# Kernel tuning notes

Hardware: AMD Instinct MI355X
Metric: run time of the kernel (lower is better)

## Reference

```python
import jax, jax.numpy as jnp
import numpy as np

CLIP_TANH = 10.0
M_CHECKS, N_VARS = 256, 512   # parity-check matrix shape
ROW_W = 8                     # ones per check row -> E = 256*8 = 2048 edges
BATCH = 16384


def _build_masks():
    """Tanner-graph connectivity masks, as in init_w_skipconn2even / initialize_w_v2c."""
    rng = np.random.default_rng(0)
    pcm = np.zeros((M_CHECKS, N_VARS), np.float32)
    for r in range(M_CHECKS):
        pcm[r, rng.choice(N_VARS, ROW_W, replace=False)] = 1.0
    checks, variables = np.nonzero(pcm)  # edge list, row-major order, length E
    E = checks.size
    # edge e' feeds edge e iff same variable node, different check node
    same_var = variables[:, None] == variables[None, :]
    diff_chk = checks[:, None] != checks[None, :]
    w_odd2even_mask = (same_var & diff_chk).astype(np.float32)               # [E, E]
    # variable v feeds every edge incident to it
    w_skip_mask = (np.arange(N_VARS)[:, None] == variables[None, :]).astype(np.float32)  # [N, E]
    return jnp.asarray(w_odd2even_mask), jnp.asarray(w_skip_mask), E


def setup_inputs() -> dict:
    key = jax.random.key(0)
    w_o2e_mask, w_skip_mask, E = _build_masks()
    k = jax.random.split(key, 5)
    return {
        "x": jax.random.normal(k[0], (BATCH, E), jnp.float32),          # edge messages
        "llr": jax.random.normal(k[1], (BATCH, N_VARS), jnp.float32),   # channel LLRs
        "u": jax.random.uniform(k[2], (E,), jnp.float32),               # dropout uniforms
        "odd_weights": 0.05 * jax.random.normal(k[3], (E, E), jnp.float32),
        "llr_weights": 1.0 + 0.05 * jax.random.normal(k[4], (N_VARS, E), jnp.float32),
        "dropout_logits": 10.0 * jnp.ones((E,), jnp.float32),           # 10000*LOGITS_INIT analogue (sigmoid ~ 1)
        "w_odd2even_mask": w_o2e_mask,
        "w_skipconn2even_mask": w_skip_mask,
    }


def reference(x, llr, u, odd_weights, llr_weights, dropout_logits,
              w_odd2even_mask, w_skipconn2even_mask):
    # TEST-phase forward, mask_only=False
    total_mask = w_odd2even_mask * odd_weights                        # [E, E], very sparse support
    z = (u < jax.nn.sigmoid(dropout_logits)).astype(x.dtype)          # Bernoulli gate per source edge
    mask_after_dropout = total_mask * z[:, None]                      # row-wise gating
    msg = x @ mask_after_dropout                                      # [B, E]
    skip = llr @ (w_skipconn2even_mask * llr_weights)                 # [B, E]
    odd_clamp = jnp.clip(msg + skip, -CLIP_TANH, CLIP_TANH)
    return jnp.tanh(0.5 * odd_clamp)
```

## Files before the change

### kernel.cpp

```cpp
#include <hip/hip_runtime.h>
#include <hip/hip_bf16.h>

constexpr int E     = 2048;
constexpr int NVARS = 512;
constexpr int DMAX  = 20;
constexpr int TB    = 8;
constexpr int NT    = 512;

__device__ __forceinline__ unsigned bf16hi(float f) {
    const unsigned uu = __float_as_uint(f);
    return (uu + 0x7FFFu + ((uu >> 16) & 1u)) & 0xFFFF0000u;
}
__device__ __forceinline__ unsigned cvtpk(float lo, float hi) {
    unsigned r;
    asm("v_cvt_pk_bf16_f32 %0, %1, %2" : "=v"(r) : "v"(lo), "v"(hi));
    return r;
}
__device__ __forceinline__ float bl(unsigned q) { return __uint_as_float(q << 16); }
__device__ __forceinline__ float bh(unsigned q) { return __uint_as_float(q & 0xFFFF0000u); }

__global__ __launch_bounds__(256)
void k_vsrc(const float* __restrict__ skip_mask,
            const float* __restrict__ llr_w,
            unsigned short* __restrict__ vsrc,
            float* __restrict__ skw)
{
    const int col = blockIdx.x * 256 + threadIdx.x;
    const int v0  = blockIdx.y * (NVARS / 32);
    for (int v = v0; v < v0 + NVARS / 32; ++v) {
        const float m = skip_mask[(size_t)v * E + col];
        if (m != 0.0f) {
            vsrc[col] = (unsigned short)v;
            skw [col] = m * llr_w[(size_t)v * E + col];
        }
    }
}

__global__ __launch_bounds__(64)
void k_pervar(const unsigned short* __restrict__ vsrc,
              const float* __restrict__ skw,
              const float* __restrict__ odd_w,
              const float* __restrict__ u,
              const float* __restrict__ logits,
              uint4*  __restrict__ wtc,
              float4* __restrict__ hdr,
              int*    __restrict__ nitems)
{
    __shared__ unsigned short vs[E];
    __shared__ int deg[NVARS];
    __shared__ unsigned short mem[DMAX];
    __shared__ float zf[DMAX];
    __shared__ float sks[DMAX];

    const int v   = blockIdx.x;
    const int tid = threadIdx.x;

    for (int i = tid; i < E / 8; i += 64)
        ((uint4*)vs)[i] = ((const uint4*)vsrc)[i];
    for (int i = tid; i < NVARS; i += 64) deg[i] = 0;
    __syncthreads();
    for (int i = tid; i < E; i += 64) atomicAdd(&deg[vs[i]], 1);
    __syncthreads();

    const int dv = deg[v];

    int itot = 0, ib = 0, wb = 0;
    for (int i = tid; i < NVARS; i += 64) {
        const int d2 = deg[i];
        if (!d2) continue;
        const int dc = (d2 < DMAX) ? d2 : DMAX;
        const int ic = (dc + 3) >> 2;
        itot += ic;
        if (dv > 0 && (d2 < dv || (d2 == dv && i < v))) { ib += ic; wb += dc * ic; }
    }
    #pragma unroll
    for (int o = 32; o; o >>= 1) {
        itot += __shfl_xor(itot, o);
        ib   += __shfl_xor(ib,   o);
        wb   += __shfl_xor(wb,   o);
    }
    if (v == 0 && tid == 0) nitems[0] = itot;
    if (!dv) return;
    const int de = (dv < DMAX) ? dv : DMAX;
    const int ic = (de + 3) >> 2;

    int cnt = 0;
    for (int c = 0; c < E / 64; ++c) {
        const int e = c * 64 + tid;
        const bool m = ((int)vs[e] == v);
        const unsigned long long bal = __ballot(m);
        if (m) {
            const int pos = cnt + __popcll(bal & ((1ull << tid) - 1ull));
            if (pos < DMAX) mem[pos] = (unsigned short)e;
        }
        cnt += __popcll(bal);
    }
    __syncthreads();

    if (tid < de) {
        const int m = mem[tid];
        const float sig = 1.0f / (1.0f + __expf(-logits[m]));
        zf [tid] = (u[m] < sig) ? 1.0f : 0.0f;
        sks[tid] = skw[m];
    }
    __syncthreads();

    if (tid < ic) {
        const int o0 = tid * 4;
        float s0 = 0, s1 = 0, s2 = 0, s3 = 0;
        unsigned c0 = 0xFFFFu, c1 = 0xFFFFu, c2 = 0xFFFFu, c3 = 0xFFFFu;
        if (o0 + 0 < de) { s0 = sks[o0 + 0]; c0 = mem[o0 + 0]; }
        if (o0 + 1 < de) { s1 = sks[o0 + 1]; c1 = mem[o0 + 1]; }
        if (o0 + 2 < de) { s2 = sks[o0 + 2]; c2 = mem[o0 + 2]; }
        if (o0 + 3 < de) { s3 = sks[o0 + 3]; c3 = mem[o0 + 3]; }
        hdr[2 * (ib + tid)]     = make_float4(s0, s1, s2, s3);
        hdr[2 * (ib + tid) + 1] = make_float4(
            __uint_as_float(c0 | (c1 << 16)),
            __uint_as_float(c2 | (c3 << 16)),
            __uint_as_float((unsigned)(wb + tid * de)),
            __uint_as_float((unsigned)v | ((unsigned)de << 16)));
    }

    for (int idx = tid; idx < de * ic; idx += 64) {
        const int k = idx / de;
        const int j = idx - k * de;
        const int src = mem[j];
        unsigned g[4];
        #pragma unroll
        for (int q = 0; q < 4; ++q) {
            const int o = 4 * k + q;
            float ww = 0.0f;
            if (o < de && o != j)
                ww = odd_w[(size_t)src * E + mem[o]] * zf[j];
            g[q] = bf16hi(ww) | (unsigned)src;
        }
        wtc[wb + idx] = make_uint4(g[0], g[1], g[2], g[3]);
    }
}

__device__ __forceinline__ float th(float s) {
    float c = fminf(fmaxf(s, -10.0f), 10.0f);
    float t = __expf(c);
    return (t - 1.0f) * __builtin_amdgcn_rcpf(t + 1.0f);
}

#define FMA8(gq, xvq)                                                         \
    {                                                                         \
        const float w0 = bh((gq).x), w1 = bh((gq).y);                         \
        const float w2 = bh((gq).z), w3 = bh((gq).w);                         \
        const float xf0 = bl((xvq).x), xf1 = bh((xvq).x);                     \
        const float xf2 = bl((xvq).y), xf3 = bh((xvq).y);                     \
        const float xf4 = bl((xvq).z), xf5 = bh((xvq).z);                     \
        const float xf6 = bl((xvq).w), xf7 = bh((xvq).w);                     \
        a[0][0] += w0 * xf0; a[0][1] += w0 * xf1;                             \
        a[0][2] += w0 * xf2; a[0][3] += w0 * xf3;                             \
        a[0][4] += w0 * xf4; a[0][5] += w0 * xf5;                             \
        a[0][6] += w0 * xf6; a[0][7] += w0 * xf7;                             \
        a[1][0] += w1 * xf0; a[1][1] += w1 * xf1;                             \
        a[1][2] += w1 * xf2; a[1][3] += w1 * xf3;                             \
        a[1][4] += w1 * xf4; a[1][5] += w1 * xf5;                             \
        a[1][6] += w1 * xf6; a[1][7] += w1 * xf7;                             \
        a[2][0] += w2 * xf0; a[2][1] += w2 * xf1;                             \
        a[2][2] += w2 * xf2; a[2][3] += w2 * xf3;                             \
        a[2][4] += w2 * xf4; a[2][5] += w2 * xf5;                             \
        a[2][6] += w2 * xf6; a[2][7] += w2 * xf7;                             \
        a[3][0] += w3 * xf0; a[3][1] += w3 * xf1;                             \
        a[3][2] += w3 * xf2; a[3][3] += w3 * xf3;                             \
        a[3][4] += w3 * xf4; a[3][5] += w3 * xf5;                             \
        a[3][6] += w3 * xf6; a[3][7] += w3 * xf7;                             \
    }

__global__ __launch_bounds__(NT, 6)
void fused_main(const float* __restrict__ x,
                const float* __restrict__ llr,
                const uint4*  __restrict__ wtc,
                const float4* __restrict__ hdr,
                const int*    __restrict__ nitems,
                float* __restrict__ out)
{
    __shared__ uint4 xs[E];
    __shared__ uint4 ls[NVARS];

    const int b0 = blockIdx.x * TB;
    const int t  = threadIdx.x;
    const int nit = nitems[0];

    const float4* xr = (const float4*)(x + (size_t)b0 * E);
    const float4 r0 = xr[0 * (E / 4) + t];
    const float4 r1 = xr[1 * (E / 4) + t];
    const float4 r2 = xr[2 * (E / 4) + t];
    const float4 r3 = xr[3 * (E / 4) + t];
    const float4 r4 = xr[4 * (E / 4) + t];
    const float4 r5 = xr[5 * (E / 4) + t];
    const float4 r6 = xr[6 * (E / 4) + t];
    const float4 r7 = xr[7 * (E / 4) + t];
    const float* lr = llr + (size_t)b0 * NVARS;
    const float l0 = lr[t],             l1 = lr[NVARS + t];
    const float l2 = lr[2 * NVARS + t], l3 = lr[3 * NVARS + t];
    const float l4 = lr[4 * NVARS + t], l5 = lr[5 * NVARS + t];
    const float l6 = lr[6 * NVARS + t], l7 = lr[7 * NVARS + t];

    const float4 ha0 = hdr[2 * t];
    const uint4  hb0 = ((const uint4*)hdr)[2 * t + 1];
    const uint4* wp0 = wtc + hb0.z;
    const uint4  g00 = wp0[0];
    const uint4  g01 = wp0[1];

    xs[4 * t + 0] = make_uint4(cvtpk(r0.x, r1.x), cvtpk(r2.x, r3.x),
                               cvtpk(r4.x, r5.x), cvtpk(r6.x, r7.x));
    xs[4 * t + 1] = make_uint4(cvtpk(r0.y, r1.y), cvtpk(r2.y, r3.y),
                               cvtpk(r4.y, r5.y), cvtpk(r6.y, r7.y));
    xs[4 * t + 2] = make_uint4(cvtpk(r0.z, r1.z), cvtpk(r2.z, r3.z),
                               cvtpk(r4.z, r5.z), cvtpk(r6.z, r7.z));
    xs[4 * t + 3] = make_uint4(cvtpk(r0.w, r1.w), cvtpk(r2.w, r3.w),
                               cvtpk(r4.w, r5.w), cvtpk(r6.w, r7.w));
    ls[t] = make_uint4(cvtpk(l0, l1), cvtpk(l2, l3),
                       cvtpk(l4, l5), cvtpk(l6, l7));
    __syncthreads();

    unsigned sst[2][4][4];
    unsigned scc[2][2];

    {
        const int v = hb0.w & 0xFFFF;
        const int d = hb0.w >> 16;

        const uint4 lvq = ls[v];
        const float lf0 = bl(lvq.x), lf1 = bh(lvq.x);
        const float lf2 = bl(lvq.y), lf3 = bh(lvq.y);
        const float lf4 = bl(lvq.z), lf5 = bh(lvq.z);
        const float lf6 = bl(lvq.w), lf7 = bh(lvq.w);

        float a[4][8];
        #pragma unroll
        for (int ii = 0; ii < 4; ++ii) {
            const float sk = (ii == 0) ? ha0.x : (ii == 1) ? ha0.y
                           : (ii == 2) ? ha0.z : ha0.w;
            a[ii][0] = sk * lf0; a[ii][1] = sk * lf1;
            a[ii][2] = sk * lf2; a[ii][3] = sk * lf3;
            a[ii][4] = sk * lf4; a[ii][5] = sk * lf5;
            a[ii][6] = sk * lf6; a[ii][7] = sk * lf7;
        }

        uint4 gc = g00, gn = g01;
        uint4 xc = xs[gc.x & 0x7FFu];
        for (int j = 0; j < d - 1; ++j) {
            const uint4 gf = wp0[j + 2];
            const uint4 xn = xs[gn.x & 0x7FFu];
            FMA8(gc, xc);
            gc = gn; xc = xn; gn = gf;
        }
        FMA8(gc, xc);

        scc[0][0] = hb0.x;
        scc[0][1] = hb0.y;
        #pragma unroll
        for (int ii = 0; ii < 4; ++ii) {
            sst[0][ii][0] = cvtpk(th(a[ii][0]), th(a[ii][1]));
            sst[0][ii][1] = cvtpk(th(a[ii][2]), th(a[ii][3]));
            sst[0][ii][2] = cvtpk(th(a[ii][4]), th(a[ii][5]));
            sst[0][ii][3] = cvtpk(th(a[ii][6]), th(a[ii][7]));
        }
    }

    scc[1][0] = 0xFFFFFFFFu;
    scc[1][1] = 0xFFFFFFFFu;
    if (NT + t < nit) {
        const int it = NT + t;
        const float4 ha1 = hdr[2 * it];
        const uint4  hb1 = ((const uint4*)hdr)[2 * it + 1];
        const uint4* wp1 = wtc + hb1.z;
        const int v = hb1.w & 0xFFFF;
        const int d = hb1.w >> 16;

        const uint4 lvq = ls[v];
        const float lf0 = bl(lvq.x), lf1 = bh(lvq.x);
        const float lf2 = bl(lvq.y), lf3 = bh(lvq.y);
        const float lf4 = bl(lvq.z), lf5 = bh(lvq.z);
        const float lf6 = bl(lvq.w), lf7 = bh(lvq.w);

        float a[4][8];
        #pragma unroll
        for (int ii = 0; ii < 4; ++ii) {
            const float sk = (ii == 0) ? ha1.x : (ii == 1) ? ha1.y
                           : (ii == 2) ? ha1.z : ha1.w;
            a[ii][0] = sk * lf0; a[ii][1] = sk * lf1;
            a[ii][2] = sk * lf2; a[ii][3] = sk * lf3;
            a[ii][4] = sk * lf4; a[ii][5] = sk * lf5;
            a[ii][6] = sk * lf6; a[ii][7] = sk * lf7;
        }

        uint4 gc = wp1[0], gn = wp1[1];
        uint4 xc = xs[gc.x & 0x7FFu];
        for (int j = 0; j < d - 1; ++j) {
            const uint4 gf = wp1[j + 2];
            const uint4 xn = xs[gn.x & 0x7FFu];
            FMA8(gc, xc);
            gc = gn; xc = xn; gn = gf;
        }
        FMA8(gc, xc);

        scc[1][0] = hb1.x;
        scc[1][1] = hb1.y;
        #pragma unroll
        for (int ii = 0; ii < 4; ++ii) {
            sst[1][ii][0] = cvtpk(th(a[ii][0]), th(a[ii][1]));
            sst[1][ii][1] = cvtpk(th(a[ii][2]), th(a[ii][3]));
            sst[1][ii][2] = cvtpk(th(a[ii][4]), th(a[ii][5]));
            sst[1][ii][3] = cvtpk(th(a[ii][6]), th(a[ii][7]));
        }
    }

    __syncthreads();
    unsigned* osp = (unsigned*)xs;
    #pragma unroll
    for (int r = 0; r < 2; ++r) {
        #pragma unroll
        for (int ii = 0; ii < 4; ++ii) {
            const unsigned c = (scc[r][ii >> 1] >> ((ii & 1) * 16)) & 0xFFFFu;
            if (c != 0xFFFFu) {
                osp[0 * E + c] = sst[r][ii][0];
                osp[1 * E + c] = sst[r][ii][1];
                osp[2 * E + c] = sst[r][ii][2];
                osp[3 * E + c] = sst[r][ii][3];
            }
        }
    }
    __syncthreads();

    {
        const int row = t >> 6, l = t & 63;
        const int p = row >> 1, hf = row & 1;
        float* orow = out + (size_t)(b0 + row) * E;
        const uint4* plane = (const uint4*)(osp + p * E);
        #pragma unroll
        for (int i = 0; i < 8; ++i) {
            const int q4 = i * 64 + l;
            const uint4 w4 = plane[q4];
            float4 o;
            if (hf == 0)
                o = make_float4(bl(w4.x), bl(w4.y), bl(w4.z), bl(w4.w));
            else
                o = make_float4(bh(w4.x), bh(w4.y), bh(w4.z), bh(w4.w));
            ((float4*)orow)[q4] = o;
        }
    }
}

extern "C" void kernel_launch(void* const* d_in, const int* in_sizes, int n_in,
                              void* d_out, int out_size, void* d_ws, size_t ws_size,
                              hipStream_t stream) {
    const float* x        = (const float*)d_in[0];
    const float* llr      = (const float*)d_in[1];
    const float* u        = (const float*)d_in[2];
    const float* odd_w    = (const float*)d_in[3];
    const float* llr_w    = (const float*)d_in[4];
    const float* logits   = (const float*)d_in[5];
    const float* skip_msk = (const float*)d_in[7];
    float* out = (float*)d_out;

    const int B = in_sizes[0] / E;

    char* wsb = (char*)d_ws;
    size_t off = 0;
    uint4*          wtc  = (uint4*)(wsb + off);          off += (size_t)6144 * 16;
    float4*         hdr  = (float4*)(wsb + off);         off += (size_t)1024 * 32;
    float*          skw  = (float*)(wsb + off);          off += (size_t)E * 4;
    unsigned short* vsrc = (unsigned short*)(wsb + off); off += (size_t)E * 2;
    int*            nit  = (int*)(wsb + off);            off += 16;

    k_vsrc  <<<dim3(E / 256, 32), dim3(256), 0, stream>>>(skip_msk, llr_w, vsrc, skw);
    k_pervar<<<dim3(NVARS),       dim3(64),  0, stream>>>(vsrc, skw, odd_w, u, logits,
                                                          wtc, hdr, nit);

    fused_main<<<dim3(B / TB), dim3(NT), 0, stream>>>(x, llr, wtc, hdr, nit, out);
}
```

Measured before the change: 96.74 us.

## Process two batch tiles per block and prefetch the second tile's x during compute

The grid is halved so each block handles two 8-row batch tiles in sequence. The x rows for the second tile are loaded into registers right after the first tile is staged in LDS, so that global load overlaps the first tile's gather/FMA compute. This trades occupancy and parallelism (half as many blocks, more live registers) for latency hiding. It also hardcodes the batch size (16384) instead of deriving it from the input size.

```diff
diff --git a/kernel.cpp b/kernel.cpp
--- a/kernel.cpp
+++ b/kernel.cpp
@@ -6,6 +6,8 @@
 constexpr int DMAX  = 20;
 constexpr int TB    = 8;
 constexpr int NT    = 512;
+constexpr int NTILE = 16384 / TB;
+constexpr int GRID  = NTILE / 2;
 
 __device__ __forceinline__ unsigned bf16hi(float f) {
     const unsigned uu = __float_as_uint(f);
@@ -181,169 +183,176 @@
     __shared__ uint4 xs[E];
     __shared__ uint4 ls[NVARS];
 
-    const int b0 = blockIdx.x * TB;
-    const int t  = threadIdx.x;
+    const int t   = threadIdx.x;
     const int nit = nitems[0];
 
-    const float4* xr = (const float4*)(x + (size_t)b0 * E);
-    const float4 r0 = xr[0 * (E / 4) + t];
-    const float4 r1 = xr[1 * (E / 4) + t];
-    const float4 r2 = xr[2 * (E / 4) + t];
-    const float4 r3 = xr[3 * (E / 4) + t];
-    const float4 r4 = xr[4 * (E / 4) + t];
-    const float4 r5 = xr[5 * (E / 4) + t];
-    const float4 r6 = xr[6 * (E / 4) + t];
-    const float4 r7 = xr[7 * (E / 4) + t];
-    const float* lr = llr + (size_t)b0 * NVARS;
-    const float l0 = lr[t],             l1 = lr[NVARS + t];
-    const float l2 = lr[2 * NVARS + t], l3 = lr[3 * NVARS + t];
-    const float l4 = lr[4 * NVARS + t], l5 = lr[5 * NVARS + t];
-    const float l6 = lr[6 * NVARS + t], l7 = lr[7 * NVARS + t];
-
-    const float4 ha0 = hdr[2 * t];
-    const uint4  hb0 = ((const uint4*)hdr)[2 * t + 1];
-    const uint4* wp0 = wtc + hb0.z;
-    const uint4  g00 = wp0[0];
-    const uint4  g01 = wp0[1];
-
-    xs[4 * t + 0] = make_uint4(cvtpk(r0.x, r1.x), cvtpk(r2.x, r3.x),
-                               cvtpk(r4.x, r5.x), cvtpk(r6.x, r7.x));
-    xs[4 * t + 1] = make_uint4(cvtpk(r0.y, r1.y), cvtpk(r2.y, r3.y),
-                               cvtpk(r4.y, r5.y), cvtpk(r6.y, r7.y));
-    xs[4 * t + 2] = make_uint4(cvtpk(r0.z, r1.z), cvtpk(r2.z, r3.z),
-                               cvtpk(r4.z, r5.z), cvtpk(r6.z, r7.z));
-    xs[4 * t + 3] = make_uint4(cvtpk(r0.w, r1.w), cvtpk(r2.w, r3.w),
-                               cvtpk(r4.w, r5.w), cvtpk(r6.w, r7.w));
-    ls[t] = make_uint4(cvtpk(l0, l1), cvtpk(l2, l3),
-                       cvtpk(l4, l5), cvtpk(l6, l7));
-    __syncthreads();
-
-    unsigned sst[2][4][4];
-    unsigned scc[2][2];
-
+    float4 rx[8];
     {
-        const int v = hb0.w & 0xFFFF;
-        const int d = hb0.w >> 16;
-
-        const uint4 lvq = ls[v];
-        const float lf0 = bl(lvq.x), lf1 = bh(lvq.x);
-        const float lf2 = bl(lvq.y), lf3 = bh(lvq.y);
-        const float lf4 = bl(lvq.z), lf5 = bh(lvq.z);
-        const float lf6 = bl(lvq.w), lf7 = bh(lvq.w);
-
-        float a[4][8];
+        const float4* xr = (const float4*)(x + (size_t)blockIdx.x * TB * E);
         #pragma unroll
-        for (int ii = 0; ii < 4; ++ii) {
-            const float sk = (ii == 0) ? ha0.x : (ii == 1) ? ha0.y
-                           : (ii == 2) ? ha0.z : ha0.w;
-            a[ii][0] = sk * lf0; a[ii][1] = sk * lf1;
-            a[ii][2] = sk * lf2; a[ii][3] = sk * lf3;
-            a[ii][4] = sk * lf4; a[ii][5] = sk * lf5;
-            a[ii][6] = sk * lf6; a[ii][7] = sk * lf7;
-        }
-
-        uint4 gc = g00, gn = g01;
-        uint4 xc = xs[gc.x & 0x7FFu];
-        for (int j = 0; j < d - 1; ++j) {
-            const uint4 gf = wp0[j + 2];
-            const uint4 xn = xs[gn.x & 0x7FFu];
+        for (int i = 0; i < 8; ++i) rx[i] = xr[i * (E / 4) + t];
+    }
+
+    #pragma unroll 1
+    for (int rep = 0; rep < 2; ++rep) {
+        const int b0 = (blockIdx.x + rep * GRID) * TB;
+
+        const float* lr = llr + (size_t)b0 * NVARS;
+        const float rl0 = lr[t],             rl1 = lr[NVARS + t];
+        const float rl2 = lr[2 * NVARS + t], rl3 = lr[3 * NVARS + t];
+        const float rl4 = lr[4 * NVARS + t], rl5 = lr[5 * NVARS + t];
+        const float rl6 = lr[6 * NVARS + t], rl7 = lr[7 * NVARS + t];
+
+        xs[4 * t + 0] = make_uint4(cvtpk(rx[0].x, rx[1].x), cvtpk(rx[2].x, rx[3].x),
+                                   cvtpk(rx[4].x, rx[5].x), cvtpk(rx[6].x, rx[7].x));
+        xs[4 * t + 1] = make_uint4(cvtpk(rx[0].y, rx[1].y), cvtpk(rx[2].y, rx[3].y),
+                                   cvtpk(rx[4].y, rx[5].y), cvtpk(rx[6].y, rx[7].y));
+        xs[4 * t + 2] = make_uint4(cvtpk(rx[0].z, rx[1].z), cvtpk(rx[2].z, rx[3].z),
+                                   cvtpk(rx[4].z, rx[5].z), cvtpk(rx[6].z, rx[7].z));
+        xs[4 * t + 3] = make_uint4(cvtpk(rx[0].w, rx[1].w), cvtpk(rx[2].w, rx[3].w),
+                                   cvtpk(rx[4].w, rx[5].w), cvtpk(rx[6].w, rx[7].w));
+        ls[t] = make_uint4(cvtpk(rl0, rl1), cvtpk(rl2, rl3),
+                           cvtpk(rl4, rl5), cvtpk(rl6, rl7));
+        __syncthreads();
+
+        if (rep == 0) {
+            const float4* xr2 = (const float4*)(x + (size_t)(b0 + GRID * TB) * E);
+            #pragma unroll
+            for (int i = 0; i < 8; ++i) rx[i] = xr2[i * (E / 4) + t];
+            __builtin_amdgcn_sched_barrier(0);
+        }
+
+        unsigned sst[2][4][4];
+        unsigned scc[2][2];
+
+        {
+            const float4 ha0 = hdr[2 * t];
+            const uint4  hb0 = ((const uint4*)hdr)[2 * t + 1];
+            const uint4* wp0 = wtc + hb0.z;
+            const int v = hb0.w & 0xFFFF;
+            const int d = hb0.w >> 16;
+
+            const uint4 lvq = ls[v];
+            const float lf0 = bl(lvq.x), lf1 = bh(lvq.x);
+            const float lf2 = bl(lvq.y), lf3 = bh(lvq.y);
+            const float lf4 = bl(lvq.z), lf5 = bh(lvq.z);
+            const float lf6 = bl(lvq.w), lf7 = bh(lvq.w);
+
+            float a[4][8];
+            #pragma unroll
+            for (int ii = 0; ii < 4; ++ii) {
+                const float sk = (ii == 0) ? ha0.x : (ii == 1) ? ha0.y
+                               : (ii == 2) ? ha0.z : ha0.w;
+                a[ii][0] = sk * lf0; a[ii][1] = sk * lf1;
+                a[ii][2] = sk * lf2; a[ii][3] = sk * lf3;
+                a[ii][4] = sk * lf4; a[ii][5] = sk * lf5;
+                a[ii][6] = sk * lf6; a[ii][7] = sk * lf7;
+            }
+
+            uint4 gc = wp0[0], gn = wp0[1];
+            uint4 xc = xs[gc.x & 0x7FFu];
+            for (int j = 0; j < d - 1; ++j) {
+                const uint4 gf = wp0[j + 2];
+                const uint4 xn = xs[gn.x & 0x7FFu];
+                FMA8(gc, xc);
+                gc = gn; xc = xn; gn = gf;
+            }
             FMA8(gc, xc);
-            gc = gn; xc = xn; gn = gf;
-        }
-        FMA8(gc, xc);
-
-        scc[0][0] = hb0.x;
-        scc[0][1] = hb0.y;
+
+            scc[0][0] = hb0.x;
+            scc[0][1] = hb0.y;
+            #pragma unroll
+            for (int ii = 0; ii < 4; ++ii) {
+                sst[0][ii][0] = cvtpk(th(a[ii][0]), th(a[ii][1]));
+                sst[0][ii][1] = cvtpk(th(a[ii][2]), th(a[ii][3]));
+                sst[0][ii][2] = cvtpk(th(a[ii][4]), th(a[ii][5]));
+                sst[0][ii][3] = cvtpk(th(a[ii][6]), th(a[ii][7]));
+            }
+        }
+
+        scc[1][0] = 0xFFFFFFFFu;
+        scc[1][1] = 0xFFFFFFFFu;
+        if (NT + t < nit) {
+            const int it = NT + t;
+            const float4 ha1 = hdr[2 * it];
+            const uint4  hb1 = ((const uint4*)hdr)[2 * it + 1];
+            const uint4* wp1 = wtc + hb1.z;
+            const int v = hb1.w & 0xFFFF;
+            const int d = hb1.w >> 16;
+
+            const uint4 lvq = ls[v];
+            const float lf0 = bl(lvq.x), lf1 = bh(lvq.x);
+            const float lf2 = bl(lvq.y), lf3 = bh(lvq.y);
+            const float lf4 = bl(lvq.z), lf5 = bh(lvq.z);
+            const float lf6 = bl(lvq.w), lf7 = bh(lvq.w);
+
+            float a[4][8];
+            #pragma unroll
+            for (int ii = 0; ii < 4; ++ii) {
+                const float sk = (ii == 0) ? ha1.x : (ii == 1) ? ha1.y
+                               : (ii == 2) ? ha1.z : ha1.w;
+                a[ii][0] = sk * lf0; a[ii][1] = sk * lf1;
+                a[ii][2] = sk * lf2; a[ii][3] = sk * lf3;
+                a[ii][4] = sk * lf4; a[ii][5] = sk * lf5;
+                a[ii][6] = sk * lf6; a[ii][7] = sk * lf7;
+            }
+
+            uint4 gc = wp1[0], gn = wp1[1];
+            uint4 xc = xs[gc.x & 0x7FFu];
+            for (int j = 0; j < d - 1; ++j) {
+                const uint4 gf = wp1[j + 2];
+                const uint4 xn = xs[gn.x & 0x7FFu];
+                FMA8(gc, xc);
+                gc = gn; xc = xn; gn = gf;
+            }
+            FMA8(gc, xc);
+
+            scc[1][0] = hb1.x;
+            scc[1][1] = hb1.y;
+            #pragma unroll
+            for (int ii = 0; ii < 4; ++ii) {
+                sst[1][ii][0] = cvtpk(th(a[ii][0]), th(a[ii][1]));
+                sst[1][ii][1] = cvtpk(th(a[ii][2]), th(a[ii][3]));
+                sst[1][ii][2] = cvtpk(th(a[ii][4]), th(a[ii][5]));
+                sst[1][ii][3] = cvtpk(th(a[ii][6]), th(a[ii][7]));
+            }
+        }
+
+        __syncthreads();
+        unsigned* osp = (unsigned*)xs;
         #pragma unroll
-        for (int ii = 0; ii < 4; ++ii) {
-            sst[0][ii][0] = cvtpk(th(a[ii][0]), th(a[ii][1]));
-            sst[0][ii][1] = cvtpk(th(a[ii][2]), th(a[ii][3]));
-            sst[0][ii][2] = cvtpk(th(a[ii][4]), th(a[ii][5]));
-            sst[0][ii][3] = cvtpk(th(a[ii][6]), th(a[ii][7]));
-        }
-    }
-
-    scc[1][0] = 0xFFFFFFFFu;
-    scc[1][1] = 0xFFFFFFFFu;
-    if (NT + t < nit) {
-        const int it = NT + t;
-        const float4 ha1 = hdr[2 * it];
-        const uint4  hb1 = ((const uint4*)hdr)[2 * it + 1];
-        const uint4* wp1 = wtc + hb1.z;
-        const int v = hb1.w & 0xFFFF;
-        const int d = hb1.w >> 16;
-
-        const uint4 lvq = ls[v];
-        const float lf0 = bl(lvq.x), lf1 = bh(lvq.x);
-        const float lf2 = bl(lvq.y), lf3 = bh(lvq.y);
-        const float lf4 = bl(lvq.z), lf5 = bh(lvq.z);
-        const float lf6 = bl(lvq.w), lf7 = bh(lvq.w);
-
-        float a[4][8];
-        #pragma unroll
-        for (int ii = 0; ii < 4; ++ii) {
-            const float sk = (ii == 0) ? ha1.x : (ii == 1) ? ha1.y
-                           : (ii == 2) ? ha1.z : ha1.w;
-            a[ii][0] = sk * lf0; a[ii][1] = sk * lf1;
-            a[ii][2] = sk * lf2; a[ii][3] = sk * lf3;
-            a[ii][4] = sk * lf4; a[ii][5] = sk * lf5;
-            a[ii][6] = sk * lf6; a[ii][7] = sk * lf7;
-        }
-
-        uint4 gc = wp1[0], gn = wp1[1];
-        uint4 xc = xs[gc.x & 0x7FFu];
-        for (int j = 0; j < d - 1; ++j) {
-            const uint4 gf = wp1[j + 2];
-            const uint4 xn = xs[gn.x & 0x7FFu];
-            FMA8(gc, xc);
-            gc = gn; xc = xn; gn = gf;
-        }
-        FMA8(gc, xc);
-
-        scc[1][0] = hb1.x;
-        scc[1][1] = hb1.y;
-        #pragma unroll
-        for (int ii = 0; ii < 4; ++ii) {
-            sst[1][ii][0] = cvtpk(th(a[ii][0]), th(a[ii][1]));
-            sst[1][ii][1] = cvtpk(th(a[ii][2]), th(a[ii][3]));
-            sst[1][ii][2] = cvtpk(th(a[ii][4]), th(a[ii][5]));
-            sst[1][ii][3] = cvtpk(th(a[ii][6]), th(a[ii][7]));
-        }
-    }
-
-    __syncthreads();
-    unsigned* osp = (unsigned*)xs;
-    #pragma unroll
-    for (int r = 0; r < 2; ++r) {
-        #pragma unroll
-        for (int ii = 0; ii < 4; ++ii) {
-            const unsigned c = (scc[r][ii >> 1] >> ((ii & 1) * 16)) & 0xFFFFu;
-            if (c != 0xFFFFu) {
-                osp[0 * E + c] = sst[r][ii][0];
-                osp[1 * E + c] = sst[r][ii][1];
-                osp[2 * E + c] = sst[r][ii][2];
-                osp[3 * E + c] = sst[r][ii][3];
-            }
-        }
-    }
-    __syncthreads();
-
-    {
-        const int row = t >> 6, l = t & 63;
-        const int p = row >> 1, hf = row & 1;
-        float* orow = out + (size_t)(b0 + row) * E;
-        const uint4* plane = (const uint4*)(osp + p * E);
-        #pragma unroll
-        for (int i = 0; i < 8; ++i) {
-            const int q4 = i * 64 + l;
-            const uint4 w4 = plane[q4];
-            float4 o;
-            if (hf == 0)
-                o = make_float4(bl(w4.x), bl(w4.y), bl(w4.z), bl(w4.w));
-            else
-                o = make_float4(bh(w4.x), bh(w4.y), bh(w4.z), bh(w4.w));
-            ((float4*)orow)[q4] = o;
-        }
+        for (int r = 0; r < 2; ++r) {
+            #pragma unroll
+            for (int ii = 0; ii < 4; ++ii) {
+                const unsigned c = (scc[r][ii >> 1] >> ((ii & 1) * 16)) & 0xFFFFu;
+                if (c != 0xFFFFu) {
+                    osp[0 * E + c] = sst[r][ii][0];
+                    osp[1 * E + c] = sst[r][ii][1];
+                    osp[2 * E + c] = sst[r][ii][2];
+                    osp[3 * E + c] = sst[r][ii][3];
+                }
+            }
+        }
+        __syncthreads();
+
+        {
+            const int row = t >> 6, l = t & 63;
+            const int p = row >> 1, hf = row & 1;
+            float* orow = out + (size_t)(b0 + row) * E;
+            const uint4* plane = (const uint4*)(osp + p * E);
+            #pragma unroll
+            for (int i = 0; i < 8; ++i) {
+                const int q4 = i * 64 + l;
+                const uint4 w4 = plane[q4];
+                float4 o;
+                if (hf == 0)
+                    o = make_float4(bl(w4.x), bl(w4.y), bl(w4.z), bl(w4.w));
+                else
+                    o = make_float4(bh(w4.x), bh(w4.y), bh(w4.z), bh(w4.w));
+                ((float4*)orow)[q4] = o;
+            }
+        }
+        __syncthreads();
     }
 }
 
@@ -359,8 +368,6 @@
     const float* skip_msk = (const float*)d_in[7];
     float* out = (float*)d_out;
 
-    const int B = in_sizes[0] / E;
-
     char* wsb = (char*)d_ws;
     size_t off = 0;
     uint4*          wtc  = (uint4*)(wsb + off);          off += (size_t)6144 * 16;
@@ -373,5 +380,5 @@
     k_pervar<<<dim3(NVARS),       dim3(64),  0, stream>>>(vsrc, skw, odd_w, u, logits,
                                                           wtc, hdr, nit);
 
-    fused_main<<<dim3(B / TB), dim3(NT), 0, stream>>>(x, llr, wtc, hdr, nit, out);
-}
+    fused_main<<<dim3(GRID), dim3(NT), 0, stream>>>(x, llr, wtc, hdr, nit, out);
+}
```

Result: slower. 181.5 us (+87.6%).

## Split batch tile into two halves to overlap x loads and output stores with gather

Applied to the files above, without the earlier changes.

The 8-row batch tile is processed as two 4-row halves held in separate shared buffers. Loads of the second half's x rows are issued after the first gather, and the first half's outputs are written before the second gather runs. The aim is to hide global load and store latency behind compute and to shrink the accumulator register footprint from 32 to 16 floats. In exchange, the sparse weight stream and headers are walked twice per block, and extra barriers are added.

```diff
diff --git a/kernel.cpp b/kernel.cpp
--- a/kernel.cpp
+++ b/kernel.cpp
@@ -144,31 +144,63 @@
     return (t - 1.0f) * __builtin_amdgcn_rcpf(t + 1.0f);
 }
 
-#define FMA8(gq, xvq)                                                         \
+#define FMA4(gq, xv2)                                                         \
     {                                                                         \
         const float w0 = bh((gq).x), w1 = bh((gq).y);                         \
         const float w2 = bh((gq).z), w3 = bh((gq).w);                         \
-        const float xf0 = bl((xvq).x), xf1 = bh((xvq).x);                     \
-        const float xf2 = bl((xvq).y), xf3 = bh((xvq).y);                     \
-        const float xf4 = bl((xvq).z), xf5 = bh((xvq).z);                     \
-        const float xf6 = bl((xvq).w), xf7 = bh((xvq).w);                     \
+        const float xf0 = bl((xv2).x), xf1 = bh((xv2).x);                     \
+        const float xf2 = bl((xv2).y), xf3 = bh((xv2).y);                     \
         a[0][0] += w0 * xf0; a[0][1] += w0 * xf1;                             \
         a[0][2] += w0 * xf2; a[0][3] += w0 * xf3;                             \
-        a[0][4] += w0 * xf4; a[0][5] += w0 * xf5;                             \
-        a[0][6] += w0 * xf6; a[0][7] += w0 * xf7;                             \
         a[1][0] += w1 * xf0; a[1][1] += w1 * xf1;                             \
         a[1][2] += w1 * xf2; a[1][3] += w1 * xf3;                             \
-        a[1][4] += w1 * xf4; a[1][5] += w1 * xf5;                             \
-        a[1][6] += w1 * xf6; a[1][7] += w1 * xf7;                             \
         a[2][0] += w2 * xf0; a[2][1] += w2 * xf1;                             \
         a[2][2] += w2 * xf2; a[2][3] += w2 * xf3;                             \
-        a[2][4] += w2 * xf4; a[2][5] += w2 * xf5;                             \
-        a[2][6] += w2 * xf6; a[2][7] += w2 * xf7;                             \
         a[3][0] += w3 * xf0; a[3][1] += w3 * xf1;                             \
         a[3][2] += w3 * xf2; a[3][3] += w3 * xf3;                             \
-        a[3][4] += w3 * xf4; a[3][5] += w3 * xf5;                             \
-        a[3][6] += w3 * xf6; a[3][7] += w3 * xf7;                             \
-    }
+    }
+
+template<int HI>
+__device__ __forceinline__ void gather_item(
+    const uint2* __restrict__ xsh, const uint4* __restrict__ lsq,
+    const uint4* __restrict__ wtc, const float4 ha, const uint4 hb,
+    unsigned st[4][2])
+{
+    const uint4* wp = wtc + hb.z;
+    const int v = hb.w & 0xFFFF;
+    const int d = hb.w >> 16;
+
+    const uint4 lvq = lsq[v];
+    const unsigned lp0 = HI ? lvq.z : lvq.x;
+    const unsigned lp1 = HI ? lvq.w : lvq.y;
+    const float lf0 = bl(lp0), lf1 = bh(lp0);
+    const float lf2 = bl(lp1), lf3 = bh(lp1);
+
+    float a[4][4];
+    #pragma unroll
+    for (int ii = 0; ii < 4; ++ii) {
+        const float sk = (ii == 0) ? ha.x : (ii == 1) ? ha.y
+                       : (ii == 2) ? ha.z : ha.w;
+        a[ii][0] = sk * lf0; a[ii][1] = sk * lf1;
+        a[ii][2] = sk * lf2; a[ii][3] = sk * lf3;
+    }
+
+    uint4 gc = wp[0], gn = wp[1];
+    uint2 xc = xsh[gc.x & 0x7FFu];
+    for (int j = 0; j < d - 1; ++j) {
+        const uint4 gf = wp[j + 2];
+        const uint2 xn = xsh[gn.x & 0x7FFu];
+        FMA4(gc, xc);
+        gc = gn; xc = xn; gn = gf;
+    }
+    FMA4(gc, xc);
+
+    #pragma unroll
+    for (int ii = 0; ii < 4; ++ii) {
+        st[ii][0] = cvtpk(th(a[ii][0]), th(a[ii][1]));
+        st[ii][1] = cvtpk(th(a[ii][2]), th(a[ii][3]));
+    }
+}
 
 __global__ __launch_bounds__(NT, 6)
 void fused_main(const float* __restrict__ x,
@@ -178,7 +210,8 @@
                 const int*    __restrict__ nitems,
                 float* __restrict__ out)
 {
-    __shared__ uint4 xs[E];
+    __shared__ uint2 xsA[E];
+    __shared__ uint2 xsB[E];
     __shared__ uint4 ls[NVARS];
 
     const int b0 = blockIdx.x * TB;
@@ -190,10 +223,6 @@
     const float4 r1 = xr[1 * (E / 4) + t];
     const float4 r2 = xr[2 * (E / 4) + t];
     const float4 r3 = xr[3 * (E / 4) + t];
-    const float4 r4 = xr[4 * (E / 4) + t];
-    const float4 r5 = xr[5 * (E / 4) + t];
-    const float4 r6 = xr[6 * (E / 4) + t];
-    const float4 r7 = xr[7 * (E / 4) + t];
     const float* lr = llr + (size_t)b0 * NVARS;
     const float l0 = lr[t],             l1 = lr[NVARS + t];
     const float l2 = lr[2 * NVARS + t], l3 = lr[3 * NVARS + t];
@@ -202,146 +231,103 @@
 
     const float4 ha0 = hdr[2 * t];
     const uint4  hb0 = ((const uint4*)hdr)[2 * t + 1];
-    const uint4* wp0 = wtc + hb0.z;
-    const uint4  g00 = wp0[0];
-    const uint4  g01 = wp0[1];
-
-    xs[4 * t + 0] = make_uint4(cvtpk(r0.x, r1.x), cvtpk(r2.x, r3.x),
-                               cvtpk(r4.x, r5.x), cvtpk(r6.x, r7.x));
-    xs[4 * t + 1] = make_uint4(cvtpk(r0.y, r1.y), cvtpk(r2.y, r3.y),
-                               cvtpk(r4.y, r5.y), cvtpk(r6.y, r7.y));
-    xs[4 * t + 2] = make_uint4(cvtpk(r0.z, r1.z), cvtpk(r2.z, r3.z),
-                               cvtpk(r4.z, r5.z), cvtpk(r6.z, r7.z));
-    xs[4 * t + 3] = make_uint4(cvtpk(r0.w, r1.w), cvtpk(r2.w, r3.w),
-                               cvtpk(r4.w, r5.w), cvtpk(r6.w, r7.w));
+
+    xsA[4 * t + 0] = make_uint2(cvtpk(r0.x, r1.x), cvtpk(r2.x, r3.x));
+    xsA[4 * t + 1] = make_uint2(cvtpk(r0.y, r1.y), cvtpk(r2.y, r3.y));
+    xsA[4 * t + 2] = make_uint2(cvtpk(r0.z, r1.z), cvtpk(r2.z, r3.z));
+    xsA[4 * t + 3] = make_uint2(cvtpk(r0.w, r1.w), cvtpk(r2.w, r3.w));
     ls[t] = make_uint4(cvtpk(l0, l1), cvtpk(l2, l3),
                        cvtpk(l4, l5), cvtpk(l6, l7));
     __syncthreads();
 
-    unsigned sst[2][4][4];
-    unsigned scc[2][2];
+    unsigned st0[4][2], st1[4][2];
+    unsigned scc0x = hb0.x, scc0y = hb0.y;
+    unsigned scc1x = 0xFFFFFFFFu, scc1y = 0xFFFFFFFFu;
+
+    gather_item<0>(xsA, ls, wtc, ha0, hb0, st0);
+
+    const float4 s4 = xr[4 * (E / 4) + t];
+    const float4 s5 = xr[5 * (E / 4) + t];
+    const float4 s6 = xr[6 * (E / 4) + t];
+    const float4 s7 = xr[7 * (E / 4) + t];
+    __builtin_amdgcn_sched_barrier(0);
+
+    const bool valid1 = (NT + t < nit);
+    float4 ha1; uint4 hb1;
+    if (valid1) {
+        ha1 = hdr[2 * (NT + t)];
+        hb1 = ((const uint4*)hdr)[2 * (NT + t) + 1];
+        scc1x = hb1.x; scc1y = hb1.y;
+        gather_item<0>(xsA, ls, wtc, ha1, hb1, st1);
+    }
+
+    __syncthreads();
+
+    xsB[4 * t + 0] = make_uint2(cvtpk(s4.x, s5.x), cvtpk(s6.x, s7.x));
+    xsB[4 * t + 1] = make_uint2(cvtpk(s4.y, s5.y), cvtpk(s6.y, s7.y));
+    xsB[4 * t + 2] = make_uint2(cvtpk(s4.z, s5.z), cvtpk(s6.z, s7.z));
+    xsB[4 * t + 3] = make_uint2(cvtpk(s4.w, s5.w), cvtpk(s6.w, s7.w));
+
+    unsigned* ospA = (unsigned*)xsA;
+    #pragma unroll
+    for (int ii = 0; ii < 4; ++ii) {
+        const unsigned c = ((ii < 2 ? scc0x : scc0y) >> ((ii & 1) * 16)) & 0xFFFFu;
+        if (c != 0xFFFFu) { ospA[c] = st0[ii][0]; ospA[E + c] = st0[ii][1]; }
+    }
+    #pragma unroll
+    for (int ii = 0; ii < 4; ++ii) {
+        const unsigned c = ((ii < 2 ? scc1x : scc1y) >> ((ii & 1) * 16)) & 0xFFFFu;
+        if (c != 0xFFFFu) { ospA[c] = st1[ii][0]; ospA[E + c] = st1[ii][1]; }
+    }
+    __syncthreads();
 
     {
-        const int v = hb0.w & 0xFFFF;
-        const int d = hb0.w >> 16;
-
-        const uint4 lvq = ls[v];
-        const float lf0 = bl(lvq.x), lf1 = bh(lvq.x);
-        const float lf2 = bl(lvq.y), lf3 = bh(lvq.y);
-        const float lf4 = bl(lvq.z), lf5 = bh(lvq.z);
-        const float lf6 = bl(lvq.w), lf7 = bh(lvq.w);
-
-        float a[4][8];
-        #pragma unroll
-        for (int ii = 0; ii < 4; ++ii) {
-            const float sk = (ii == 0) ? ha0.x : (ii == 1) ? ha0.y
-                           : (ii == 2) ? ha0.z : ha0.w;
-            a[ii][0] = sk * lf0; a[ii][1] = sk * lf1;
-            a[ii][2] = sk * lf2; a[ii][3] = sk * lf3;
-            a[ii][4] = sk * lf4; a[ii][5] = sk * lf5;
-            a[ii][6] = sk * lf6; a[ii][7] = sk * lf7;
-        }
-
-        uint4 gc = g00, gn = g01;
-        uint4 xc = xs[gc.x & 0x7FFu];
-        for (int j = 0; j < d - 1; ++j) {
-            const uint4 gf = wp0[j + 2];
-            const uint4 xn = xs[gn.x & 0x7FFu];
-            FMA8(gc, xc);
-            gc = gn; xc = xn; gn = gf;
-        }
-        FMA8(gc, xc);
-
-        scc[0][0] = hb0.x;
-        scc[0][1] = hb0.y;
-        #pragma unroll
-        for (int ii = 0; ii < 4; ++ii) {
-            sst[0][ii][0] = cvtpk(th(a[ii][0]), th(a[ii][1]));
-            sst[0][ii][1] = cvtpk(th(a[ii][2]), th(a[ii][3]));
-            sst[0][ii][2] = cvtpk(th(a[ii][4]), th(a[ii][5]));
-            sst[0][ii][3] = cvtpk(th(a[ii][6]), th(a[ii][7]));
-        }
-    }
-
-    scc[1][0] = 0xFFFFFFFFu;
-    scc[1][1] = 0xFFFFFFFFu;
-    if (NT + t < nit) {
-        const int it = NT + t;
-        const float4 ha1 = hdr[2 * it];
-        const uint4  hb1 = ((const uint4*)hdr)[2 * it + 1];
-        const uint4* wp1 = wtc + hb1.z;
-        const int v = hb1.w & 0xFFFF;
-        const int d = hb1.w >> 16;
-
-        const uint4 lvq = ls[v];
-        const float lf0 = bl(lvq.x), lf1 = bh(lvq.x);
-        const float lf2 = bl(lvq.y), lf3 = bh(lvq.y);
-        const float lf4 = bl(lvq.z), lf5 = bh(lvq.z);
-        const float lf6 = bl(lvq.w), lf7 = bh(lvq.w);
-
-        float a[4][8];
-        #pragma unroll
-        for (int ii = 0; ii < 4; ++ii) {
-            const float sk = (ii == 0) ? ha1.x : (ii == 1) ? ha1.y
-                           : (ii == 2) ? ha1.z : ha1.w;
-            a[ii][0] = sk * lf0; a[ii][1] = sk * lf1;
-            a[ii][2] = sk * lf2; a[ii][3] = sk * lf3;
-            a[ii][4] = sk * lf4; a[ii][5] = sk * lf5;
-            a[ii][6] = sk * lf6; a[ii][7] = sk * lf7;
-        }
-
-        uint4 gc = wp1[0], gn = wp1[1];
-        uint4 xc = xs[gc.x & 0x7FFu];
-        for (int j = 0; j < d - 1; ++j) {
-            const uint4 gf = wp1[j + 2];
-            const uint4 xn = xs[gn.x & 0x7FFu];
-            FMA8(gc, xc);
-            gc = gn; xc = xn; gn = gf;
-        }
-        FMA8(gc, xc);
-
-        scc[1][0] = hb1.x;
-        scc[1][1] = hb1.y;
-        #pragma unroll
-        for (int ii = 0; ii < 4; ++ii) {
-            sst[1][ii][0] = cvtpk(th(a[ii][0]), th(a[ii][1]));
-            sst[1][ii][1] = cvtpk(th(a[ii][2]), th(a[ii][3]));
-            sst[1][ii][2] = cvtpk(th(a[ii][4]), th(a[ii][5]));
-            sst[1][ii][3] = cvtpk(th(a[ii][6]), th(a[ii][7]));
-        }
-    }
-
-    __syncthreads();
-    unsigned* osp = (unsigned*)xs;
-    #pragma unroll
-    for (int r = 0; r < 2; ++r) {
-        #pragma unroll
-        for (int ii = 0; ii < 4; ++ii) {
-            const unsigned c = (scc[r][ii >> 1] >> ((ii & 1) * 16)) & 0xFFFFu;
-            if (c != 0xFFFFu) {
-                osp[0 * E + c] = sst[r][ii][0];
-                osp[1 * E + c] = sst[r][ii][1];
-                osp[2 * E + c] = sst[r][ii][2];
-                osp[3 * E + c] = sst[r][ii][3];
-            }
-        }
-    }
-    __syncthreads();
-
-    {
-        const int row = t >> 6, l = t & 63;
+        const int row = t >> 7, l = t & 127;
         const int p = row >> 1, hf = row & 1;
         float* orow = out + (size_t)(b0 + row) * E;
-        const uint4* plane = (const uint4*)(osp + p * E);
+        const uint4* pl = (const uint4*)(ospA + p * E);
         #pragma unroll
-        for (int i = 0; i < 8; ++i) {
-            const int q4 = i * 64 + l;
-            const uint4 w4 = plane[q4];
+        for (int i = 0; i < 4; ++i) {
+            const int q4 = i * 128 + l;
+            const uint4 w4 = pl[q4];
             float4 o;
-            if (hf == 0)
-                o = make_float4(bl(w4.x), bl(w4.y), bl(w4.z), bl(w4.w));
-            else
-                o = make_float4(bh(w4.x), bh(w4.y), bh(w4.z), bh(w4.w));
+            if (hf == 0) o = make_float4(bl(w4.x), bl(w4.y), bl(w4.z), bl(w4.w));
+            else         o = make_float4(bh(w4.x), bh(w4.y), bh(w4.z), bh(w4.w));
+            ((float4*)orow)[q4] = o;
+        }
+    }
+
+    gather_item<1>(xsB, ls, wtc, ha0, hb0, st0);
+    if (valid1)
+        gather_item<1>(xsB, ls, wtc, ha1, hb1, st1);
+
+    __syncthreads();
+
+    unsigned* ospB = (unsigned*)xsB;
+    #pragma unroll
+    for (int ii = 0; ii < 4; ++ii) {
+        const unsigned c = ((ii < 2 ? scc0x : scc0y) >> ((ii & 1) * 16)) & 0xFFFFu;
+        if (c != 0xFFFFu) { ospB[c] = st0[ii][0]; ospB[E + c] = st0[ii][1]; }
+    }
+    #pragma unroll
+    for (int ii = 0; ii < 4; ++ii) {
+        const unsigned c = ((ii < 2 ? scc1x : scc1y) >> ((ii & 1) * 16)) & 0xFFFFu;
+        if (c != 0xFFFFu) { ospB[c] = st1[ii][0]; ospB[E + c] = st1[ii][1]; }
+    }
+    __syncthreads();
+
+    {
+        const int row = t >> 7, l = t & 127;
+        const int p = row >> 1, hf = row & 1;
+        float* orow = out + (size_t)(b0 + 4 + row) * E;
+        const uint4* pl = (const uint4*)(ospB + p * E);
+        #pragma unroll
+        for (int i = 0; i < 4; ++i) {
+            const int q4 = i * 128 + l;
+            const uint4 w4 = pl[q4];
+            float4 o;
+            if (hf == 0) o = make_float4(bl(w4.x), bl(w4.y), bl(w4.z), bl(w4.w));
+            else         o = make_float4(bh(w4.x), bh(w4.y), bh(w4.z), bh(w4.w));
             ((float4*)orow)[q4] = o;
         }
     }
```

Result: slower. 135.7 us (+40.3%).
